# Performance work log

Hardware: AMD Instinct MI355X
Metric: run time of the kernel (lower is better)

The kernel has to match this reference:

```python
import jax, jax.numpy as jnp
import numpy as np

B, T, E, D, G = 64, 64, 2048, 4096, 8
H3 = 3 * D  # gru projects deter -> 3*deter (reset, cand, update)
EPS = 1e-4  # Norm default eps


def _rms(x, scale):
    # Norm impl='rms': x * rsqrt(mean(x^2, -1) + eps) * scale
    return x * (jax.lax.rsqrt((x * x).mean(-1, keepdims=True) + EPS) * scale)


def setup_inputs() -> dict:
    key = jax.random.key(0)
    ks = jax.random.split(key, 4)
    x = jax.random.normal(ks[0], (B, T, E), jnp.float32)
    deter0 = jax.random.normal(ks[1], (B, D), jnp.float32)
    # dense in-projection: concat(deter, x) -> D, rms norm + silu
    W_in = jax.random.normal(ks[2], (D + E, D), jnp.float32) * (1.0 / np.sqrt(D + E))
    b_in = jnp.zeros((D,), jnp.float32)
    scale_in = jnp.ones((D,), jnp.float32)
    # BlockLinear D -> 3D with G groups; weight (G, D/G, 3D/G), per-block rms scales
    W_blk = jax.random.normal(ks[3], (G, D // G, H3 // G), jnp.float32) * (1.0 / np.sqrt(D // G))
    b_blk = jnp.zeros((H3,), jnp.float32)
    scale_blk = jnp.ones((G, H3 // G), jnp.float32)
    return dict(x=x, deter0=deter0, W_in=W_in, b_in=b_in, scale_in=scale_in,
                W_blk=W_blk, b_blk=b_blk, scale_blk=scale_blk)


def reference(x, deter0, W_in, b_in, scale_in, W_blk, b_blk, scale_blk):
    def step(deter, x_t):
        h = jnp.concatenate([deter, x_t], -1)                # [B, D+E]
        y = jax.nn.silu(_rms(h @ W_in + b_in, scale_in))     # [B, D]
        # block-diagonal GEMM: '...ki,kio->...ko' as in BlockLinear._layer
        z = jnp.einsum('bgi,gio->bgo', y.reshape(B, G, D // G), W_blk)
        z = z.reshape(B, H3) + b_blk
        # block_norm=True: per-block rms over each of the G contiguous chunks
        z = _rms(z.reshape(B, G, H3 // G), scale_blk).reshape(B, H3)
        reset, cand, update = jnp.split(z, 3, -1)
        reset = jax.nn.sigmoid(reset)
        cand = jnp.tanh(reset * cand)
        update = jax.nn.sigmoid(update - 1.0)
        deter = update * cand + (1.0 - update) * deter
        return deter, deter

    _, deters = jax.lax.scan(step, deter0, jnp.swapaxes(x, 0, 1))  # scan over T
    return jnp.swapaxes(deters, 0, 1)  # [B, T, D]
```

## Files before the change

kernel.cpp:

```cpp
#include <hip/hip_runtime.h>

typedef unsigned short u16;
typedef unsigned int u32;
typedef __bf16 bfx8 __attribute__((ext_vector_type(8)));
typedef float f32x4 __attribute__((ext_vector_type(4)));

constexpr int BB = 64;
constexpr int TT = 64;
constexpr int EE = 2048;
constexpr int DD = 4096;
constexpr int GG = 8;
constexpr int H3 = 3 * DD;
constexpr int CH = H3 / GG;
constexpr float EPSf = 1e-4f;

static __device__ __forceinline__ u16 f2bf(float f) {
  u32 u = __builtin_bit_cast(u32, f);
  u32 r = (u + 0x7fffu + ((u >> 16) & 1u)) >> 16;
  return (u16)r;
}
static __device__ __forceinline__ float bf2f(u16 h) {
  return __builtin_bit_cast(float, (u32)h << 16);
}

#define GLOAD_LDS16(gp, lp)                                                    \
  __builtin_amdgcn_global_load_lds(                                           \
      (const __attribute__((address_space(1))) void*)(gp),                    \
      (__attribute__((address_space(3))) void*)(lp), 16, 0, 0)


__global__ void __launch_bounds__(256) k_f2b(const float* __restrict__ in,
                                             u16* __restrict__ out, int n4) {
  int i = blockIdx.x * 256 + threadIdx.x;
  int stride = gridDim.x * 256;
  for (; i < n4; i += stride) {
    float4 v = ((const float4*)in)[i];
    uint2 o;
    o.x = (u32)f2bf(v.x) | ((u32)f2bf(v.y) << 16);
    o.y = (u32)f2bf(v.z) | ((u32)f2bf(v.w) << 16);
    ((uint2*)out)[i] = o;
  }
}

__global__ void __launch_bounds__(256) k_initdet(const float* __restrict__ d0,
                                                 float* __restrict__ dF,
                                                 u16* __restrict__ dB, int n4) {
  int i = blockIdx.x * 256 + threadIdx.x;
  if (i < n4) {
    float4 v = ((const float4*)d0)[i];
    ((float4*)dF)[i] = v;
    uint2 o;
    o.x = (u32)f2bf(v.x) | ((u32)f2bf(v.y) << 16);
    o.y = (u32)f2bf(v.z) | ((u32)f2bf(v.w) << 16);
    ((uint2*)dB)[i] = o;
  }
}

__global__ void __launch_bounds__(256) k_transpose_f2b(const float* __restrict__ in,
                                                       u16* __restrict__ out,
                                                       int R, int C) {
  __shared__ float tile[32][33];
  size_t base = (size_t)blockIdx.z * R * C;
  in += base; out += base;
  int tx = threadIdx.x & 31, ty = threadIdx.x >> 5;
  int r0 = blockIdx.y * 32, c0 = blockIdx.x * 32;
#pragma unroll
  for (int i = 0; i < 4; i++) {
    int rr = ty * 4 + i;
    tile[rr][tx] = in[(size_t)(r0 + rr) * C + (c0 + tx)];
  }
  __syncthreads();
#pragma unroll
  for (int i = 0; i < 4; i++) {
    int cc = ty * 4 + i;
    out[(size_t)(c0 + cc) * R + (r0 + tx)] = f2bf(tile[tx][cc]);
  }
}


__global__ void __launch_bounds__(256) k_p1(const u16* __restrict__ A,
                                            const u16* __restrict__ B,
                                            const float* __restrict__ bias,
                                            u16* __restrict__ C) {
  __shared__ u16 As[128 * 64];
  __shared__ u16 Bs[128 * 64];
  const int tid = threadIdx.x;
  const int m0 = blockIdx.y * 128, n0 = blockIdx.x * 128;
  const int w = tid >> 6, lane = tid & 63;
  const int wr = w >> 1, wc = w & 1;
  const int lr = lane & 15, lk = (lane >> 4) * 8;
  const int lrow = lane >> 3;
  const int lcol = (lane & 7) * 8;
  const u16* gA[4];
  const u16* gB[4];
  u16* lA[4];
  u16* lB[4];
#pragma unroll
  for (int i = 0; i < 4; i++) {
    const int chunk = w * 4 + i;
    const int row = chunk * 8 + lrow;
    gA[i] = A + (size_t)(m0 + row) * EE + lcol;
    gB[i] = B + (size_t)(n0 + row) * (DD + EE) + lcol;
    lA[i] = &As[chunk * 512];
    lB[i] = &Bs[chunk * 512];
  }

  f32x4 acc[4][4] = {};

  for (int kt = 0; kt < EE; kt += 64) {
#pragma unroll
    for (int i = 0; i < 4; i++) {
      GLOAD_LDS16(gA[i] + kt, lA[i]);
      GLOAD_LDS16(gB[i] + kt, lB[i]);
    }
    __syncthreads();
#pragma unroll
    for (int kk = 0; kk < 64; kk += 32) {
      bfx8 av[4], bv[4];
#pragma unroll
      for (int mi = 0; mi < 4; mi++)
        av[mi] = *(const bfx8*)&As[(wr * 64 + mi * 16 + lr) * 64 + kk + lk];
#pragma unroll
      for (int ni = 0; ni < 4; ni++)
        bv[ni] = *(const bfx8*)&Bs[(wc * 64 + ni * 16 + lr) * 64 + kk + lk];
#pragma unroll
      for (int mi = 0; mi < 4; mi++)
#pragma unroll
        for (int ni = 0; ni < 4; ni++)
          acc[mi][ni] = __builtin_amdgcn_mfma_f32_16x16x32_bf16(av[mi], bv[ni], acc[mi][ni], 0, 0, 0);
    }
    __syncthreads();
  }

  const int rq = (lane >> 4) * 4;
#pragma unroll
  for (int mi = 0; mi < 4; mi++) {
#pragma unroll
    for (int ni = 0; ni < 4; ni++) {
      const int n = n0 + wc * 64 + ni * 16 + lr;
      const float bias_v = bias[n];
#pragma unroll
      for (int r = 0; r < 4; r++) {
        const int m = m0 + wr * 64 + mi * 16 + rq + r;
        C[(size_t)m * DD + n] = f2bf(acc[mi][ni][r] + bias_v);
      }
    }
  }
}

constexpr int LSA = 136;
constexpr int ABUF = 64 * LSA;

__global__ void __launch_bounds__(512) kA(const u16* __restrict__ dB,
                                          const u16* __restrict__ WT,
                                          float* __restrict__ part) {
  __shared__ u16 As[2 * ABUF];
  __shared__ u16 Bs[2 * ABUF];
  const int tid = threadIdx.x;
  const int n0 = blockIdx.x * 64;
  const int k0 = blockIdx.y * 1024;
  const int w = tid >> 6, lane = tid & 63;
  const int wr = w >> 1, wc = w & 1;
  const int lr = lane & 15, lk = (lane >> 4) * 8, rq = (lane >> 4) * 4;
  const int r0s = tid >> 4, s0 = (tid & 15) * 8;
  const int r1s = r0s + 32;
  const u16* Ag0 = dB + (size_t)r0s * DD + k0 + s0;
  const u16* Ag1 = dB + (size_t)r1s * DD + k0 + s0;
  const u16* Bg0 = WT + (size_t)(n0 + r0s) * (DD + EE) + k0 + s0;
  const u16* Bg1 = WT + (size_t)(n0 + r1s) * (DD + EE) + k0 + s0;
  const int d0 = r0s * LSA + s0, d1 = r1s * LSA + s0;

  f32x4 acc[2] = {};
  uint4 ra0 = *(const uint4*)(Ag0);
  uint4 ra1 = *(const uint4*)(Ag1);
  uint4 rb0 = *(const uint4*)(Bg0);
  uint4 rb1 = *(const uint4*)(Bg1);

  for (int kt = 0; kt < 8; ++kt) {
    const int p = kt & 1;
    u16* ab = As + p * ABUF;
    u16* bb = Bs + p * ABUF;
    *(uint4*)&ab[d0] = ra0;
    *(uint4*)&ab[d1] = ra1;
    *(uint4*)&bb[d0] = rb0;
    *(uint4*)&bb[d1] = rb1;
    __syncthreads();
    if (kt < 7) {
      const int ko = (kt + 1) * 128;
      ra0 = *(const uint4*)(Ag0 + ko);
      ra1 = *(const uint4*)(Ag1 + ko);
      rb0 = *(const uint4*)(Bg0 + ko);
      rb1 = *(const uint4*)(Bg1 + ko);
    }
#pragma unroll
    for (int kk = 0; kk < 128; kk += 32) {
      bfx8 av = *(const bfx8*)&ab[(wr * 16 + lr) * LSA + kk + lk];
#pragma unroll
      for (int ni = 0; ni < 2; ni++) {
        bfx8 bv = *(const bfx8*)&bb[(wc * 32 + ni * 16 + lr) * LSA + kk + lk];
        acc[ni] = __builtin_amdgcn_mfma_f32_16x16x32_bf16(av, bv, acc[ni], 0, 0, 0);
      }
    }
  }

  float* Pp = part + (size_t)blockIdx.y * BB * DD;
#pragma unroll
  for (int ni = 0; ni < 2; ni++)
#pragma unroll
    for (int r = 0; r < 4; r++)
      Pp[(size_t)(wr * 16 + rq + r) * DD + n0 + wc * 32 + ni * 16 + lr] = acc[ni][r];
}

__global__ void __launch_bounds__(256) kB(const float* __restrict__ part,
                                          const u16* __restrict__ Xproj,
                                          const float* __restrict__ scale_in,
                                          u16* __restrict__ ybf, int t) {
  const int b = blockIdx.x, tid = threadIdx.x;
  const int w = tid >> 6, lane = tid & 63;
  __shared__ float sred[4];
  const u16* xp = Xproj + ((size_t)b * TT + t) * DD + tid * 16;
  const float* pb = part + (size_t)b * DD + tid * 16;
  float v[16];
  uint4 x0 = *(const uint4*)(xp);
  uint4 x1 = *(const uint4*)(xp + 8);
#pragma unroll
  for (int j = 0; j < 8; j++) {
    v[j] = bf2f(((const u16*)&x0)[j]);
    v[8 + j] = bf2f(((const u16*)&x1)[j]);
  }
#pragma unroll
  for (int kc = 0; kc < 4; kc++) {
    const float* p = pb + (size_t)kc * BB * DD;
#pragma unroll
    for (int j4 = 0; j4 < 4; j4++) {
      float4 q = *(const float4*)(p + j4 * 4);
      v[j4 * 4 + 0] += q.x; v[j4 * 4 + 1] += q.y;
      v[j4 * 4 + 2] += q.z; v[j4 * 4 + 3] += q.w;
    }
  }
  float ss = 0.f;
#pragma unroll
  for (int j = 0; j < 16; j++) ss += v[j] * v[j];
#pragma unroll
  for (int o = 32; o > 0; o >>= 1) ss += __shfl_down(ss, o);
  if (lane == 0) sred[w] = ss;
  __syncthreads();
  const float r = rsqrtf((sred[0] + sred[1] + sred[2] + sred[3]) / (float)DD + EPSf);
  const float* sc = scale_in + tid * 16;
  u32 pk[8];
#pragma unroll
  for (int j = 0; j < 8; j++) {
    float a = v[2 * j] * r * sc[2 * j];
    float bq = v[2 * j + 1] * r * sc[2 * j + 1];
    a = a / (1.f + __expf(-a));
    bq = bq / (1.f + __expf(-bq));
    pk[j] = (u32)f2bf(a) | ((u32)f2bf(bq) << 16);
  }
  *(uint4*)(ybf + (size_t)b * DD + tid * 16) = make_uint4(pk[0], pk[1], pk[2], pk[3]);
  *(uint4*)(ybf + (size_t)b * DD + tid * 16 + 8) = make_uint4(pk[4], pk[5], pk[6], pk[7]);
}

constexpr int LSC2 = 72;
constexpr int CBUF = 64 * LSC2;

__global__ void __launch_bounds__(256) kC(const u16* __restrict__ ybf,
                                          const u16* __restrict__ WbT,
                                          const float* __restrict__ b_blk,
                                          float* __restrict__ zbuf,
                                          float* __restrict__ zsq) {
  __shared__ u16 As[2 * CBUF];
  __shared__ u16 Bs[2 * CBUF];
  const int tid = threadIdx.x;
  const int wg = blockIdx.x;
  const int n0g = wg * 64;
  const int g = n0g / CH, nl = n0g % CH;
  const int w = tid >> 6, lane = tid & 63;
  const int lr = lane & 15, lk = (lane >> 4) * 8, rq = (lane >> 4) * 4;
  const int srow = tid >> 2, sc = (tid & 3) * 8;
  const u16* Arow = ybf + (size_t)srow * DD + g * (DD / GG) + sc;
  const u16* Brow = WbT + ((size_t)g * CH + nl + srow) * (DD / GG) + sc;
  const int dA = srow * LSC2 + sc;

  f32x4 acc[4] = {};
  uint4 ra0 = *(const uint4*)(Arow);
  uint4 ra1 = *(const uint4*)(Arow + 32);
  uint4 rb0 = *(const uint4*)(Brow);
  uint4 rb1 = *(const uint4*)(Brow + 32);

  for (int kt = 0; kt < 8; ++kt) {
    const int p = kt & 1;
    u16* ab = As + p * CBUF;
    u16* bb = Bs + p * CBUF;
    *(uint4*)&ab[dA] = ra0;
    *(uint4*)&ab[dA + 32] = ra1;
    *(uint4*)&bb[dA] = rb0;
    *(uint4*)&bb[dA + 32] = rb1;
    __syncthreads();
    if (kt < 7) {
      const int ko = (kt + 1) * 64;
      ra0 = *(const uint4*)(Arow + ko);
      ra1 = *(const uint4*)(Arow + ko + 32);
      rb0 = *(const uint4*)(Brow + ko);
      rb1 = *(const uint4*)(Brow + ko + 32);
    }
#pragma unroll
    for (int kk = 0; kk < 64; kk += 32) {
      bfx8 av = *(const bfx8*)&ab[(w * 16 + lr) * LSC2 + kk + lk];
#pragma unroll
      for (int ni = 0; ni < 4; ni++) {
        bfx8 bv = *(const bfx8*)&bb[(ni * 16 + lr) * LSC2 + kk + lk];
        acc[ni] = __builtin_amdgcn_mfma_f32_16x16x32_bf16(av, bv, acc[ni], 0, 0, 0);
      }
    }
  }

  float sq[4] = {0.f, 0.f, 0.f, 0.f};
#pragma unroll
  for (int ni = 0; ni < 4; ni++) {
    const int n = n0g + ni * 16 + lr;
    const float bias_v = b_blk[n];
#pragma unroll
    for (int r = 0; r < 4; r++) {
      const float zv = acc[ni][r] + bias_v;
      zbuf[(size_t)(w * 16 + rq + r) * H3 + n] = zv;
      sq[r] += zv * zv;
    }
  }
#pragma unroll
  for (int o = 1; o < 16; o <<= 1) {
#pragma unroll
    for (int r = 0; r < 4; r++) sq[r] += __shfl_xor(sq[r], o);
  }
  if (lr == 0) {
#pragma unroll
    for (int r = 0; r < 4; r++) zsq[(size_t)wg * 64 + w * 16 + rq + r] = sq[r];
  }
}

__global__ void __launch_bounds__(256) kD(const float* __restrict__ zbuf,
                                          const float* __restrict__ zsq,
                                          const float* __restrict__ sblk,
                                          float* __restrict__ dF,
                                          u16* __restrict__ dB,
                                          float* __restrict__ out, int t) {
  const int wg = blockIdx.x, tid = threadIdx.x;
  const int b = wg >> 2, s = wg & 3;
  __shared__ float sred[8];
  if (tid < 8) {
    float ssq = 0.f;
    const int j0 = tid * 24;
#pragma unroll
    for (int j = 0; j < 24; j++) ssq += zsq[(size_t)(j0 + j) * 64 + b];
    sred[tid] = rsqrtf(ssq / (float)CH + EPSf);
  }
  __syncthreads();
  const int d0 = s * 1024 + tid * 4;
  const float* zr = zbuf + (size_t)b * H3;
  float4 z0 = *(const float4*)(zr + d0);
  float4 z1 = *(const float4*)(zr + DD + d0);
  float4 z2 = *(const float4*)(zr + 2 * DD + d0);
  float4 dold = *(const float4*)(dF + (size_t)b * DD + d0);
  const float rsA = sred[d0 / CH];
  const float rsB = sred[(DD + d0) / CH];
  const float rsC = sred[(2 * DD + d0) / CH];
  float dn[4];
  const float* z0p = (const float*)&z0;
  const float* z1p = (const float*)&z1;
  const float* z2p = (const float*)&z2;
  const float* dop = (const float*)&dold;
#pragma unroll
  for (int e = 0; e < 4; e++) {
    const int dd = d0 + e;
    const float a0 = z0p[e] * rsA * sblk[dd];
    const float a1 = z1p[e] * rsB * sblk[DD + dd];
    const float a2 = z2p[e] * rsC * sblk[2 * DD + dd];
    const float reset = 1.f / (1.f + __expf(-a0));
    const float cand = tanhf(reset * a1);
    const float upd = 1.f / (1.f + __expf(-(a2 - 1.f)));
    dn[e] = upd * cand + (1.f - upd) * dop[e];
  }
  *(float4*)(dF + (size_t)b * DD + d0) = make_float4(dn[0], dn[1], dn[2], dn[3]);
  uint2 o;
  o.x = (u32)f2bf(dn[0]) | ((u32)f2bf(dn[1]) << 16);
  o.y = (u32)f2bf(dn[2]) | ((u32)f2bf(dn[3]) << 16);
  *(uint2*)(dB + (size_t)b * DD + d0) = o;
  *(float4*)(out + ((size_t)b * TT + t) * DD + d0) = make_float4(dn[0], dn[1], dn[2], dn[3]);
}


extern "C" void kernel_launch(void* const* d_in, const int* in_sizes, int n_in,
                              void* d_out, int out_size, void* d_ws, size_t ws_size,
                              hipStream_t stream) {
  (void)in_sizes; (void)n_in; (void)out_size; (void)ws_size;
  const float* x         = (const float*)d_in[0];
  const float* deter0    = (const float*)d_in[1];
  const float* W_in      = (const float*)d_in[2];
  const float* b_in      = (const float*)d_in[3];
  const float* scale_in  = (const float*)d_in[4];
  const float* W_blk     = (const float*)d_in[5];
  const float* b_blk     = (const float*)d_in[6];
  const float* scale_blk = (const float*)d_in[7];
  float* out = (float*)d_out;

  char* ws = (char*)d_ws;
  size_t off = 0;
  auto alloc = [&](size_t bytes) -> void* {
    void* p = ws + off;
    off += (bytes + 255) & ~(size_t)255;
    return p;
  };
  u16*   WT    = (u16*)alloc((size_t)DD * (DD + EE) * 2);
  u16*   WbT   = (u16*)alloc((size_t)GG * CH * (DD / GG) * 2);
  u16*   Xproj = (u16*)alloc((size_t)BB * TT * DD * 2);
  float* dF    = (float*)alloc((size_t)BB * DD * 4);
  u16*   dB    = (u16*)alloc((size_t)BB * DD * 2);
  char* scratch = (char*)alloc((size_t)BB * TT * EE * 2);
  u16*   xbf  = (u16*)scratch;
  float* part = (float*)scratch;
  size_t o2 = (size_t)4 * BB * DD * 4;
  u16*   ybf  = (u16*)(scratch + o2);
  o2 += (size_t)BB * DD * 2;
  float* zbuf = (float*)(scratch + o2);
  o2 += (size_t)BB * H3 * 4;
  float* zsq  = (float*)(scratch + o2);

  k_f2b<<<dim3(2048), dim3(256), 0, stream>>>(x, xbf, BB * TT * EE / 4);
  k_transpose_f2b<<<dim3(DD / 32, (DD + EE) / 32, 1), dim3(256), 0, stream>>>(W_in, WT, DD + EE, DD);
  k_transpose_f2b<<<dim3(CH / 32, (DD / GG) / 32, GG), dim3(256), 0, stream>>>(W_blk, WbT, DD / GG, CH);
  k_initdet<<<dim3(BB * DD / 4 / 256), dim3(256), 0, stream>>>(deter0, dF, dB, BB * DD / 4);

  k_p1<<<dim3(DD / 128, BB * TT / 128), dim3(256), 0, stream>>>(
      xbf, WT + DD, b_in, Xproj);

  for (int t = 0; t < TT; t++) {
    kA<<<dim3(64, 4), dim3(512), 0, stream>>>(dB, WT, part);
    kB<<<dim3(BB), dim3(256), 0, stream>>>(part, Xproj, scale_in, ybf, t);
    kC<<<dim3(192), dim3(256), 0, stream>>>(ybf, WbT, b_blk, zbuf, zsq);
    kD<<<dim3(256), dim3(256), 0, stream>>>(zbuf, zsq, scale_blk, dF, dB, out, t);
  }
}
```

Measured before the change: 1.800 ms.

## Use swizzled direct-to-LDS loads in recurrent GEMMs and widen RMS-norm kernel

The input-projection GEMM (k_p1) now XOR-swizzles its LDS layout so the MFMA fragment reads avoid bank conflicts. The per-step recurrent GEMM (kA) replaces register-staged, padded LDS stores with swizzled direct global-to-LDS async loads, double-buffered so the next tile is fetched while the current one is consumed. The RMS-norm/SiLU kernel (kB) doubles its threads per row, processing 8 elements per thread instead of 16. The aim is to cut LDS bank conflicts and register staging on the serial 64-step critical path. The risk is that the swizzle must match exactly between load and read, and the async-load double buffering depends on correct sync placement.

```diff
diff --git a/kernel.cpp b/kernel.cpp
--- a/kernel.cpp
+++ b/kernel.cpp
@@ -90,7 +90,7 @@
   const int wr = w >> 1, wc = w & 1;
   const int lr = lane & 15, lk = (lane >> 4) * 8;
   const int lrow = lane >> 3;
-  const int lcol = (lane & 7) * 8;
+  const int lcol = (((lane & 7) ^ (lane >> 3)) << 3);
   const u16* gA[4];
   const u16* gB[4];
   u16* lA[4];
@@ -116,13 +116,14 @@
     __syncthreads();
 #pragma unroll
     for (int kk = 0; kk < 64; kk += 32) {
+      const int sl = (((kk + lk) >> 3) ^ (lr & 7)) << 3;
       bfx8 av[4], bv[4];
 #pragma unroll
       for (int mi = 0; mi < 4; mi++)
-        av[mi] = *(const bfx8*)&As[(wr * 64 + mi * 16 + lr) * 64 + kk + lk];
+        av[mi] = *(const bfx8*)&As[(wr * 64 + mi * 16 + lr) * 64 + sl];
 #pragma unroll
       for (int ni = 0; ni < 4; ni++)
-        bv[ni] = *(const bfx8*)&Bs[(wc * 64 + ni * 16 + lr) * 64 + kk + lk];
+        bv[ni] = *(const bfx8*)&Bs[(wc * 64 + ni * 16 + lr) * 64 + sl];
 #pragma unroll
       for (int mi = 0; mi < 4; mi++)
 #pragma unroll
@@ -148,59 +149,60 @@
   }
 }
 
-constexpr int LSA = 136;
-constexpr int ABUF = 64 * LSA;
 
 __global__ void __launch_bounds__(512) kA(const u16* __restrict__ dB,
                                           const u16* __restrict__ WT,
                                           float* __restrict__ part) {
-  __shared__ u16 As[2 * ABUF];
-  __shared__ u16 Bs[2 * ABUF];
+  __shared__ u16 As[2 * 8192];
+  __shared__ u16 Bs[2 * 8192];
   const int tid = threadIdx.x;
   const int n0 = blockIdx.x * 64;
   const int k0 = blockIdx.y * 1024;
   const int w = tid >> 6, lane = tid & 63;
   const int wr = w >> 1, wc = w & 1;
   const int lr = lane & 15, lk = (lane >> 4) * 8, rq = (lane >> 4) * 4;
-  const int r0s = tid >> 4, s0 = (tid & 15) * 8;
-  const int r1s = r0s + 32;
-  const u16* Ag0 = dB + (size_t)r0s * DD + k0 + s0;
-  const u16* Ag1 = dB + (size_t)r1s * DD + k0 + s0;
-  const u16* Bg0 = WT + (size_t)(n0 + r0s) * (DD + EE) + k0 + s0;
-  const u16* Bg1 = WT + (size_t)(n0 + r1s) * (DD + EE) + k0 + s0;
-  const int d0 = r0s * LSA + s0, d1 = r1s * LSA + s0;
+  const int r0 = w * 4 + (lane >> 4);
+  const int r1 = r0 + 32;
+  const int s0 = (((lane & 15) ^ (r0 & 15)) << 3);
+  const int s1 = (((lane & 15) ^ (r1 & 15)) << 3);
+  const u16* gA0 = dB + (size_t)r0 * DD + k0 + s0;
+  const u16* gA1 = dB + (size_t)r1 * DD + k0 + s1;
+  const u16* gB0 = WT + (size_t)(n0 + r0) * (DD + EE) + k0 + s0;
+  const u16* gB1 = WT + (size_t)(n0 + r1) * (DD + EE) + k0 + s1;
+  u16* dA0 = &As[0] + w * 512;
+  u16* dA1 = &As[0] + 4096 + w * 512;
+  u16* dB0 = &Bs[0] + w * 512;
+  u16* dB1 = &Bs[0] + 4096 + w * 512;
 
   f32x4 acc[2] = {};
-  uint4 ra0 = *(const uint4*)(Ag0);
-  uint4 ra1 = *(const uint4*)(Ag1);
-  uint4 rb0 = *(const uint4*)(Bg0);
-  uint4 rb1 = *(const uint4*)(Bg1);
+  GLOAD_LDS16(gA0, dA0);
+  GLOAD_LDS16(gA1, dA1);
+  GLOAD_LDS16(gB0, dB0);
+  GLOAD_LDS16(gB1, dB1);
+  __syncthreads();
 
   for (int kt = 0; kt < 8; ++kt) {
-    const int p = kt & 1;
-    u16* ab = As + p * ABUF;
-    u16* bb = Bs + p * ABUF;
-    *(uint4*)&ab[d0] = ra0;
-    *(uint4*)&ab[d1] = ra1;
-    *(uint4*)&bb[d0] = rb0;
-    *(uint4*)&bb[d1] = rb1;
-    __syncthreads();
+    const int p = kt & 1, q = p ^ 1;
     if (kt < 7) {
       const int ko = (kt + 1) * 128;
-      ra0 = *(const uint4*)(Ag0 + ko);
-      ra1 = *(const uint4*)(Ag1 + ko);
-      rb0 = *(const uint4*)(Bg0 + ko);
-      rb1 = *(const uint4*)(Bg1 + ko);
-    }
+      GLOAD_LDS16(gA0 + ko, dA0 + q * 8192);
+      GLOAD_LDS16(gA1 + ko, dA1 + q * 8192);
+      GLOAD_LDS16(gB0 + ko, dB0 + q * 8192);
+      GLOAD_LDS16(gB1 + ko, dB1 + q * 8192);
+    }
+    const u16* ab = &As[p * 8192];
+    const u16* bb = &Bs[p * 8192];
 #pragma unroll
     for (int kk = 0; kk < 128; kk += 32) {
-      bfx8 av = *(const bfx8*)&ab[(wr * 16 + lr) * LSA + kk + lk];
+      const int sl = ((((kk + lk) >> 3)) ^ lr) << 3;
+      bfx8 av = *(const bfx8*)&ab[(wr * 16 + lr) * 128 + sl];
 #pragma unroll
       for (int ni = 0; ni < 2; ni++) {
-        bfx8 bv = *(const bfx8*)&bb[(wc * 32 + ni * 16 + lr) * LSA + kk + lk];
+        bfx8 bv = *(const bfx8*)&bb[(wc * 32 + ni * 16 + lr) * 128 + sl];
         acc[ni] = __builtin_amdgcn_mfma_f32_16x16x32_bf16(av, bv, acc[ni], 0, 0, 0);
       }
     }
+    __syncthreads();
   }
 
   float* Pp = part + (size_t)blockIdx.y * BB * DD;
@@ -211,53 +213,49 @@
       Pp[(size_t)(wr * 16 + rq + r) * DD + n0 + wc * 32 + ni * 16 + lr] = acc[ni][r];
 }
 
-__global__ void __launch_bounds__(256) kB(const float* __restrict__ part,
+__global__ void __launch_bounds__(512) kB(const float* __restrict__ part,
                                           const u16* __restrict__ Xproj,
                                           const float* __restrict__ scale_in,
                                           u16* __restrict__ ybf, int t) {
   const int b = blockIdx.x, tid = threadIdx.x;
   const int w = tid >> 6, lane = tid & 63;
-  __shared__ float sred[4];
-  const u16* xp = Xproj + ((size_t)b * TT + t) * DD + tid * 16;
-  const float* pb = part + (size_t)b * DD + tid * 16;
-  float v[16];
+  __shared__ float sred[8];
+  const u16* xp = Xproj + ((size_t)b * TT + t) * DD + tid * 8;
+  const float* pb = part + (size_t)b * DD + tid * 8;
+  float v[8];
   uint4 x0 = *(const uint4*)(xp);
-  uint4 x1 = *(const uint4*)(xp + 8);
-#pragma unroll
-  for (int j = 0; j < 8; j++) {
-    v[j] = bf2f(((const u16*)&x0)[j]);
-    v[8 + j] = bf2f(((const u16*)&x1)[j]);
-  }
+#pragma unroll
+  for (int j = 0; j < 8; j++) v[j] = bf2f(((const u16*)&x0)[j]);
 #pragma unroll
   for (int kc = 0; kc < 4; kc++) {
     const float* p = pb + (size_t)kc * BB * DD;
-#pragma unroll
-    for (int j4 = 0; j4 < 4; j4++) {
-      float4 q = *(const float4*)(p + j4 * 4);
-      v[j4 * 4 + 0] += q.x; v[j4 * 4 + 1] += q.y;
-      v[j4 * 4 + 2] += q.z; v[j4 * 4 + 3] += q.w;
-    }
+    float4 q0 = *(const float4*)(p);
+    float4 q1 = *(const float4*)(p + 4);
+    v[0] += q0.x; v[1] += q0.y; v[2] += q0.z; v[3] += q0.w;
+    v[4] += q1.x; v[5] += q1.y; v[6] += q1.z; v[7] += q1.w;
   }
   float ss = 0.f;
 #pragma unroll
-  for (int j = 0; j < 16; j++) ss += v[j] * v[j];
+  for (int j = 0; j < 8; j++) ss += v[j] * v[j];
 #pragma unroll
   for (int o = 32; o > 0; o >>= 1) ss += __shfl_down(ss, o);
   if (lane == 0) sred[w] = ss;
   __syncthreads();
-  const float r = rsqrtf((sred[0] + sred[1] + sred[2] + sred[3]) / (float)DD + EPSf);
-  const float* sc = scale_in + tid * 16;
-  u32 pk[8];
-#pragma unroll
-  for (int j = 0; j < 8; j++) {
+  float tot = 0.f;
+#pragma unroll
+  for (int i = 0; i < 8; i++) tot += sred[i];
+  const float r = rsqrtf(tot / (float)DD + EPSf);
+  const float* sc = scale_in + tid * 8;
+  u32 pk[4];
+#pragma unroll
+  for (int j = 0; j < 4; j++) {
     float a = v[2 * j] * r * sc[2 * j];
     float bq = v[2 * j + 1] * r * sc[2 * j + 1];
     a = a / (1.f + __expf(-a));
     bq = bq / (1.f + __expf(-bq));
     pk[j] = (u32)f2bf(a) | ((u32)f2bf(bq) << 16);
   }
-  *(uint4*)(ybf + (size_t)b * DD + tid * 16) = make_uint4(pk[0], pk[1], pk[2], pk[3]);
-  *(uint4*)(ybf + (size_t)b * DD + tid * 16 + 8) = make_uint4(pk[4], pk[5], pk[6], pk[7]);
+  *(uint4*)(ybf + (size_t)b * DD + tid * 8) = make_uint4(pk[0], pk[1], pk[2], pk[3]);
 }
 
 constexpr int LSC2 = 72;
@@ -434,7 +432,7 @@
 
   for (int t = 0; t < TT; t++) {
     kA<<<dim3(64, 4), dim3(512), 0, stream>>>(dB, WT, part);
-    kB<<<dim3(BB), dim3(256), 0, stream>>>(part, Xproj, scale_in, ybf, t);
+    kB<<<dim3(BB), dim3(512), 0, stream>>>(part, Xproj, scale_in, ybf, t);
     kC<<<dim3(192), dim3(256), 0, stream>>>(ybf, WbT, b_blk, zbuf, zsq);
     kD<<<dim3(256), dim3(256), 0, stream>>>(zbuf, zsq, scale_blk, dF, dB, out, t);
   }
```

After: 1.766 ms (median of 2 runs). About the same (-1.9%).
